# Optimization experiments

Hardware: AMD Instinct MI355X
Metric: run time of the kernel (lower is better)

Reference implementation:

```python
import jax, jax.numpy as jnp
import numpy as np

EPS = 1e-4

def _softmax_features(x, proj, is_query):
    # x: [B,H,N,D], proj: [M,D] -> features [B,H,N,M] (FAVOR+ softmax kernel)
    d = x.shape[-1]
    m = proj.shape[0]
    data_normalizer = d ** -0.25
    ratio = m ** -0.5
    xd = jnp.einsum('bhnd,md->bhnm', x * data_normalizer, proj)
    diag = 0.5 * (data_normalizer ** 2) * jnp.sum(x * x, axis=-1, keepdims=True)  # [B,H,N,1]
    if is_query:
        mx = jax.lax.stop_gradient(jnp.max(xd, axis=-1, keepdims=True))
    else:
        mx = jax.lax.stop_gradient(jnp.max(xd, axis=(-1, -2), keepdims=True))
    return ratio * (jnp.exp(xd - diag - mx) + EPS)

def setup_inputs() -> dict:
    key = jax.random.key(0)
    kq, kk, kv, kp = jax.random.split(key, 4)
    B, H, N, D, M = 4, 8, 8192, 64, 256
    Q = jax.random.normal(kq, (B, H, N, D), dtype=jnp.float32)
    K = jax.random.normal(kk, (B, H, N, D), dtype=jnp.float32)
    V = jax.random.normal(kv, (B, H, N, D), dtype=jnp.float32)
    mask = jnp.ones((B, N), dtype=jnp.float32)
    proj = jax.random.normal(kp, (M, D), dtype=jnp.float32)
    return {'Q': Q, 'K': K, 'V': V, 'mask': mask, 'proj': proj}

def reference(Q, K, V, mask, proj):
    # Mask keys/values before the kernel, as in the torch module
    Km = K * mask[:, None, :, None]
    Vm = V * mask[:, None, :, None]
    q = _softmax_features(Q, proj, is_query=True)    # [B,H,N,M]
    k = _softmax_features(Km, proj, is_query=False)  # [B,H,N,M]
    # Non-causal linear attention: out = q (k^T v) / (q k_sum)
    k_sum = jnp.sum(k, axis=-2)                         # [B,H,M]
    d_inv = 1.0 / jnp.einsum('bhnm,bhm->bhn', q, k_sum)  # [B,H,N]
    ctx = jnp.einsum('bhnm,bhnd->bhmd', k, Vm)            # [B,H,M,D]
    out = jnp.einsum('bhnm,bhmd,bhn->bhnd', q, ctx, d_inv)
    return out
```

## Files before the change

kernel.cpp:

```cpp
#include <hip/hip_runtime.h>


typedef __attribute__((ext_vector_type(8))) short short8;
typedef __attribute__((ext_vector_type(8))) _Float16 half8;
typedef __attribute__((ext_vector_type(4))) float f32x4;

namespace {
constexpr int BN = 8192, DD = 64, MM = 256, NHEADS = 32;
constexpr float CNORM = 0.35355339059327373f;
constexpr float LOG2E = 1.4426950408889634f;
constexpr float DGC   = 0.34657359027997264f;
constexpr float FEPS  = 1e-4f;
constexpr float INV2048 = 4.8828125e-4f;
constexpr int FFS = 260;

constexpr size_t OFF_BX    = 0;
constexpr size_t OFF_CS    = 8192;
constexpr size_t OFF_KSUMP = 270336;
constexpr size_t OFF_KSUMG = 335872;
constexpr size_t OFF_VSP   = 344320;
constexpr size_t OFF_CTXP  = 360704;
}

__device__ __forceinline__ unsigned short f2bf(float f) {
  unsigned u = __float_as_uint(f);
  u += 0x7fffu + ((u >> 16) & 1u);
  return (unsigned short)(u >> 16);
}
__device__ __forceinline__ float bf2f(unsigned short h) {
  return __uint_as_float(((unsigned)h) << 16);
}
__device__ __forceinline__ unsigned pk2(unsigned short a, unsigned short b) {
  return (unsigned)a | ((unsigned)b << 16);
}
__device__ __forceinline__ unsigned short f2h(float f) {
  _Float16 h = (_Float16)f;
  return __builtin_bit_cast(unsigned short, h);
}
__device__ __forceinline__ float exp2hw(float x) {
  float r;
  asm("v_exp_f32 %0, %1" : "=v"(r) : "v"(x));
  return r;
}
__device__ __forceinline__ unsigned cvtpk(float lo, float hi) {
  unsigned r;
  asm("v_cvt_pk_bf16_f32 %0, %1, %2" : "=v"(r) : "v"(lo), "v"(hi));
  return r;
}

template <int T>
__device__ __forceinline__ void xcd_map(int& bh, int& tile) {
  int id = blockIdx.y * T + blockIdx.x;
  int xcd = id & 7, s = id >> 3;
  bh = xcd * 4 + s / T;
  tile = s % T;
}

__global__ void kPrep(const float* __restrict__ proj, unsigned short* __restrict__ BxG) {
  int s = blockIdx.x * 256 + threadIdx.x;
  int l = s & 63, kb = (s >> 6) & 1, mt = s >> 7;
  int n = mt * 16 + (l & 15);
  int k0 = kb * 32 + (l >> 4) * 8;
  unsigned short o[8];
#pragma unroll
  for (int j = 0; j < 8; ++j) o[j] = f2h(proj[n * 64 + k0 + j]);
  *(uint4*)(BxG + (size_t)s * 8) =
      make_uint4(pk2(o[0], o[1]), pk2(o[2], o[3]), pk2(o[4], o[5]), pk2(o[6], o[7]));
}

__global__ void __launch_bounds__(512, 4)
kCtx(const float* __restrict__ Kin, const float* __restrict__ Vin,
     const float* __restrict__ mask, const unsigned short* __restrict__ BxG,
     float* __restrict__ ctxp, float* __restrict__ ksump,
     float* __restrict__ mxg, float* __restrict__ vsp) {
  __shared__ __align__(16) unsigned short BxH[8192];
  __shared__ __align__(16) unsigned short Fs[128 * 140];
  __shared__ __align__(16) unsigned short VF[16 * 64 * 8];
  __shared__ float wmax[8];
  __shared__ float ksred[1024];
  __shared__ float vred[512];
  const int tid = threadIdx.x;
  int bh, tl16;
  xcd_map<16>(bh, tl16);
  const int tile = tl16 >> 1, mh = tl16 & 1;
  const int b = bh >> 3;
  const float* Kh = Kin + (size_t)bh * BN * DD;
  const float* Vh = Vin + (size_t)bh * BN * DD;
  const float* mrow = mask + (size_t)b * BN;
#pragma unroll
  for (int i = 0; i < 2; ++i)
    ((uint4*)BxH)[tid + i * 512] = ((const uint4*)BxG)[mh * 1024 + tid + i * 512];
  const int w = tid >> 6, l = tid & 63, lm = l & 15, kl = l >> 4;
  const int lmv = tid & 15, klnv = (tid >> 4) & 3, dtv = (tid >> 6) & 3, ksv0 = tid >> 8;

  f32x4 cacc[4];
#pragma unroll
  for (int dt = 0; dt < 4; ++dt) cacc[dt] = f32x4{0.f, 0.f, 0.f, 0.f};
  float kspart[8] = {0.f, 0.f, 0.f, 0.f, 0.f, 0.f, 0.f, 0.f};
  float wm = -3e38f, vsum = 0.f;

  const int rbase = tile * 1024;
  float4 kv0, kv1, kv2, kv3;
  float mskK;
  {
    const float* rp = Kh + (size_t)(rbase + w * 16 + lm) * 64 + kl * 8;
    kv0 = *(const float4*)rp;        kv1 = *(const float4*)(rp + 4);
    kv2 = *(const float4*)(rp + 32); kv3 = *(const float4*)(rp + 36);
    mskK = mrow[rbase + w * 16 + lm];
  }
  __syncthreads();

  for (int ch = 0; ch < 8; ++ch) {
    const int r0 = rbase + ch * 128;
    half8 ah0, ah1, al0, al1;
    float diagv;
    {
      float scale = CNORM * LOG2E * mskK;
      float x[16] = {kv0.x, kv0.y, kv0.z, kv0.w, kv1.x, kv1.y, kv1.z, kv1.w,
                     kv2.x, kv2.y, kv2.z, kv2.w, kv3.x, kv3.y, kv3.z, kv3.w};
      float sq = 0.f;
#pragma unroll
      for (int e = 0; e < 16; ++e) {
        float y = x[e] * scale;
        _Float16 h = (_Float16)y;
        _Float16 lo = (_Float16)((y - (float)h) * 2048.0f);
        if (e < 8) { ah0[e] = h; al0[e] = lo; } else { ah1[e - 8] = h; al1[e - 8] = lo; }
        sq = fmaf(y, y, sq);
      }
      sq += __shfl_xor(sq, 16);
      sq += __shfl_xor(sq, 32);
      diagv = DGC * sq;
    }
    {
      const int nr = rbase + ((ch + 1) & 7) * 128 + w * 16 + lm;
      const float* rp = Kh + (size_t)nr * 64 + kl * 8;
      kv0 = *(const float4*)rp;        kv1 = *(const float4*)(rp + 4);
      kv2 = *(const float4*)(rp + 32); kv3 = *(const float4*)(rp + 36);
      mskK = mrow[nr];
    }
    float vv[16];
#pragma unroll
    for (int h = 0; h < 2; ++h) {
      int nb = (ksv0 * 2 + h) * 32 + klnv * 8;
#pragma unroll
      for (int j = 0; j < 8; ++j)
        vv[h * 8 + j] = Vh[(size_t)(r0 + nb + j) * 64 + dtv * 16 + lmv];
    }
    float dgv[4];
#pragma unroll
    for (int r = 0; r < 4; ++r)
      dgv[r] = __shfl(diagv, (l & 48) + kl * 4 + r);
#pragma unroll
    for (int j = 0; j < 8; ++j) {
      half8 b0 = *(const half8*)&BxH[((j * 2 + 0) * 64 + l) * 8];
      half8 b1 = *(const half8*)&BxH[((j * 2 + 1) * 64 + l) * 8];
      f32x4 a0 = {0.f, 0.f, 0.f, 0.f}, a1 = {0.f, 0.f, 0.f, 0.f};
      a0 = __builtin_amdgcn_mfma_f32_16x16x32_f16(ah0, b0, a0, 0, 0, 0);
      a0 = __builtin_amdgcn_mfma_f32_16x16x32_f16(ah1, b1, a0, 0, 0, 0);
      a1 = __builtin_amdgcn_mfma_f32_16x16x32_f16(al0, b0, a1, 0, 0, 0);
      a1 = __builtin_amdgcn_mfma_f32_16x16x32_f16(al1, b1, a1, 0, 0, 0);
      float x0 = fmaf(a1[0], INV2048, a0[0]);
      float x1 = fmaf(a1[1], INV2048, a0[1]);
      float x2 = fmaf(a1[2], INV2048, a0[2]);
      float x3 = fmaf(a1[3], INV2048, a0[3]);
      wm = fmaxf(wm, fmaxf(fmaxf(x0, x1), fmaxf(x2, x3)));
      float f0 = exp2hw(x0 - dgv[0]);
      float f1 = exp2hw(x1 - dgv[1]);
      float f2 = exp2hw(x2 - dgv[2]);
      float f3 = exp2hw(x3 - dgv[3]);
      kspart[j] += f0 + f1 + f2 + f3;
      *(uint2*)&Fs[(j * 16 + lm) * 140 + w * 16 + kl * 4] =
          make_uint2(cvtpk(f0, f1), cvtpk(f2, f3));
    }
#pragma unroll
    for (int h = 0; h < 2; ++h) {
      int ks = ksv0 * 2 + h;
      int nb = ks * 32 + klnv * 8;
      float4 m0 = *(const float4*)&mrow[r0 + nb];
      float4 m1 = *(const float4*)&mrow[r0 + nb + 4];
      float mk[8] = {m0.x, m0.y, m0.z, m0.w, m1.x, m1.y, m1.z, m1.w};
      float vm[8];
#pragma unroll
      for (int j = 0; j < 8; ++j) {
        vm[j] = vv[h * 8 + j] * mk[j];
        vsum += vm[j];
      }
      *(uint4*)&VF[((ks * 4 + dtv) * 64 + klnv * 16 + lmv) * 8] =
          make_uint4(cvtpk(vm[0], vm[1]), cvtpk(vm[2], vm[3]),
                     cvtpk(vm[4], vm[5]), cvtpk(vm[6], vm[7]));
    }
    __syncthreads();
#pragma unroll
    for (int ks = 0; ks < 4; ++ks) {
      union { short8 v; uint2 u[2]; } af;
      const int ab = (w * 16 + lm) * 140 + ks * 32 + kl * 8;
      af.u[0] = *(const uint2*)&Fs[ab];
      af.u[1] = *(const uint2*)&Fs[ab + 4];
#pragma unroll
      for (int dt = 0; dt < 4; ++dt) {
        short8 vb = *(const short8*)&VF[((ks * 4 + dt) * 64 + l) * 8];
        cacc[dt] = __builtin_amdgcn_mfma_f32_16x16x32_bf16(af.v, vb, cacc[dt], 0, 0, 0);
      }
    }
    __syncthreads();
  }
#pragma unroll
  for (int j = 0; j < 8; ++j) {
    kspart[j] += __shfl_xor(kspart[j], 16);
    kspart[j] += __shfl_xor(kspart[j], 32);
  }
  if (l < 16) {
#pragma unroll
    for (int j = 0; j < 8; ++j) ksred[(j * 16 + l) * 8 + w] = kspart[j];
  }
  {
    wm = fmaxf(wm, __shfl_xor(wm, 1));  wm = fmaxf(wm, __shfl_xor(wm, 2));
    wm = fmaxf(wm, __shfl_xor(wm, 4));  wm = fmaxf(wm, __shfl_xor(wm, 8));
    wm = fmaxf(wm, __shfl_xor(wm, 16)); wm = fmaxf(wm, __shfl_xor(wm, 32));
    if (l == 0) wmax[w] = wm;
  }
  vred[tid] = vsum;
  __syncthreads();
  if (tid < 128) {
    float s = 0.f;
#pragma unroll
    for (int k = 0; k < 8; ++k) s += ksred[tid * 8 + k];
    ksump[(size_t)(bh * 16 + tl16) * 128 + tid] = s;
  }
  if (mh == 0 && tid < 64) {
    float vs = 0.f;
#pragma unroll
    for (int k = 0; k < 8; ++k)
      vs += vred[(k >> 2) * 256 + (tid >> 4) * 64 + (k & 3) * 16 + (tid & 15)];
    vsp[(size_t)(bh * 8 + tile) * 64 + tid] = vs;
  }
  if (tid == 0) {
    float bm = wmax[0];
#pragma unroll
    for (int i = 1; i < 8; ++i) bm = fmaxf(bm, wmax[i]);
    mxg[bh * 256 + 240 + tl16] = bm;
  }
  float* cp = ctxp + (size_t)(bh * 16 + tl16) * 8192;
#pragma unroll
  for (int dt = 0; dt < 4; ++dt)
#pragma unroll
    for (int r = 0; r < 4; ++r)
      cp[(w * 16 + kl * 4 + r) * 64 + dt * 16 + lm] = cacc[dt][r];
}

__global__ void kRedCtx(const float* __restrict__ ctxp, const float* __restrict__ ksump,
                        const float* __restrict__ vsp, unsigned short* __restrict__ CsG,
                        float* __restrict__ ksumG) {
  __shared__ __align__(16) float ctxL[16384];
  __shared__ float vsL[64];
  const int bh = blockIdx.x, t = threadIdx.x;
  float MX = -3e38f;
#pragma unroll
  for (int i = 0; i < 16; ++i) MX = fmaxf(MX, ksumG[bh * 256 + 240 + i]);
  const float fsc = exp2hw(-MX);
  __syncthreads();
#pragma unroll
  for (int i = 0; i < 16; ++i) {
    int idx4 = t + i * 256;
    int mhi = (idx4 >> 11) & 1;
    int loc = idx4 & 2047;
    float4 s = make_float4(0.f, 0.f, 0.f, 0.f);
#pragma unroll
    for (int tl = 0; tl < 8; ++tl) {
      float4 a = ((const float4*)(ctxp + (size_t)(bh * 16 + tl * 2 + mhi) * 8192))[loc];
      s.x += a.x; s.y += a.y; s.z += a.z; s.w += a.w;
    }
    s.x *= fsc; s.y *= fsc; s.z *= fsc; s.w *= fsc;
    ((float4*)ctxL)[idx4] = s;
  }
  {
    int mhi = t >> 7, loc = t & 127;
    float ks = 0.f;
#pragma unroll
    for (int tl = 0; tl < 8; ++tl)
      ks += ksump[(size_t)(bh * 16 + tl * 2 + mhi) * 128 + loc];
    ksumG[bh * 256 + t] = fsc * ks + FEPS * (float)BN;
  }
  if (t < 64) {
    float vs = 0.f;
#pragma unroll
    for (int tl = 0; tl < 8; ++tl) vs += vsp[(size_t)(bh * 8 + tl) * 64 + t];
    vsL[t] = vs;
  }
  __syncthreads();
#pragma unroll
  for (int i = 0; i < 8; ++i) {
    int slot = t + i * 256;
    int l = slot & 63, s = (slot >> 6) & 7, dt = slot >> 9;
    int d = dt * 16 + (l & 15);
    int mb = s * 32 + (l >> 4) * 8;
    float ve = FEPS * vsL[d];
    unsigned short o[8];
#pragma unroll
    for (int j = 0; j < 8; ++j) o[j] = f2bf(ctxL[(mb + j) * 64 + d] + ve);
    *(uint4*)(CsG + (size_t)bh * 16384 + (size_t)slot * 8) =
        make_uint4(pk2(o[0], o[1]), pk2(o[2], o[3]), pk2(o[4], o[5]), pk2(o[6], o[7]));
  }
}

__global__ void __launch_bounds__(256, 2)
kOut(const float* __restrict__ Qin, const unsigned short* __restrict__ BxG,
     const unsigned short* __restrict__ CsG, const float* __restrict__ ksumG,
     float* __restrict__ outp) {
  __shared__ __align__(16) unsigned short BxH[16384];
  __shared__ __align__(16) unsigned short Ff[64 * FFS];
  __shared__ float den[64];
  const int tid = threadIdx.x;
  int bh, tile;
  xcd_map<32>(bh, tile);
  const float* Qh = Qin + (size_t)bh * BN * DD;
  const unsigned short* CsB = CsG + (size_t)bh * 16384;
  const int w = tid >> 6, l = tid & 63, lm = l & 15, kl = l >> 4;
#pragma unroll
  for (int i = 0; i < 16; ++i)
    ((uint4*)BxH)[tid + i * 256] = ((const uint4*)BxG)[tid + i * 256];
  short8 cb[8];
#pragma unroll
  for (int s = 0; s < 8; ++s)
    cb[s] = *(const short8*)(CsB + (size_t)(((w * 8 + s) * 64 + l) * 8));
  float kss[16];
#pragma unroll
  for (int j = 0; j < 16; ++j) kss[j] = ksumG[bh * 256 + j * 16 + lm];
  float4 qv0, qv1, qv2, qv3;
  {
    const float* rp = Qh + (size_t)(tile * 256 + w * 16 + lm) * 64 + kl * 8;
    qv0 = *(const float4*)rp;        qv1 = *(const float4*)(rp + 4);
    qv2 = *(const float4*)(rp + 32); qv3 = *(const float4*)(rp + 36);
  }
  __syncthreads();

  for (int ch = 0; ch < 4; ++ch) {
    const int r0 = tile * 256 + ch * 64;
    half8 ah0, ah1, al0, al1;
    float sq = 0.f;
    {
      const float scale = CNORM * LOG2E;
      float x[16] = {qv0.x, qv0.y, qv0.z, qv0.w, qv1.x, qv1.y, qv1.z, qv1.w,
                     qv2.x, qv2.y, qv2.z, qv2.w, qv3.x, qv3.y, qv3.z, qv3.w};
#pragma unroll
      for (int e = 0; e < 16; ++e) {
        float y = x[e] * scale;
        _Float16 h = (_Float16)y;
        _Float16 lo = (_Float16)((y - (float)h) * 2048.0f);
        if (e < 8) { ah0[e] = h; al0[e] = lo; } else { ah1[e - 8] = h; al1[e - 8] = lo; }
        sq = fmaf(y, y, sq);
      }
      sq += __shfl_xor(sq, 16);
      sq += __shfl_xor(sq, 32);
    }
    const float diagv = DGC * sq;
    {
      const int nr = tile * 256 + ((ch + 1) & 3) * 64 + w * 16 + lm;
      const float* rp = Qh + (size_t)nr * 64 + kl * 8;
      qv0 = *(const float4*)rp;        qv1 = *(const float4*)(rp + 4);
      qv2 = *(const float4*)(rp + 32); qv3 = *(const float4*)(rp + 36);
    }
    f32x4 accC[16];
#pragma unroll
    for (int j = 0; j < 16; ++j) {
      half8 b0 = *(const half8*)&BxH[((j * 2 + 0) * 64 + l) * 8];
      half8 b1 = *(const half8*)&BxH[((j * 2 + 1) * 64 + l) * 8];
      f32x4 acc0 = {0.f, 0.f, 0.f, 0.f}, acc1 = {0.f, 0.f, 0.f, 0.f};
      acc0 = __builtin_amdgcn_mfma_f32_16x16x32_f16(ah0, b0, acc0, 0, 0, 0);
      acc0 = __builtin_amdgcn_mfma_f32_16x16x32_f16(ah1, b1, acc0, 0, 0, 0);
      acc1 = __builtin_amdgcn_mfma_f32_16x16x32_f16(al0, b0, acc1, 0, 0, 0);
      acc1 = __builtin_amdgcn_mfma_f32_16x16x32_f16(al1, b1, acc1, 0, 0, 0);
#pragma unroll
      for (int r = 0; r < 4; ++r) accC[j][r] = fmaf(acc1[r], INV2048, acc0[r]);
    }
    float mrow[4];
#pragma unroll
    for (int r = 0; r < 4; ++r) {
      float m0 = accC[0][r];
#pragma unroll
      for (int j = 1; j < 16; ++j) m0 = fmaxf(m0, accC[j][r]);
      m0 = fmaxf(m0, __shfl_xor(m0, 1));
      m0 = fmaxf(m0, __shfl_xor(m0, 2));
      m0 = fmaxf(m0, __shfl_xor(m0, 4));
      m0 = fmaxf(m0, __shfl_xor(m0, 8));
      mrow[r] = m0;
    }
    float dgv[4], dnn[4] = {0.f, 0.f, 0.f, 0.f};
#pragma unroll
    for (int r = 0; r < 4; ++r)
      dgv[r] = __shfl(diagv, (l & 48) + kl * 4 + r) + mrow[r];
#pragma unroll
    for (int j = 0; j < 16; ++j) {
#pragma unroll
      for (int r = 0; r < 4; ++r) {
        float q = exp2hw(accC[j][r] - dgv[r]) + FEPS;
        unsigned short qh = f2bf(q);
        Ff[(w * 16 + kl * 4 + r) * FFS + j * 16 + lm] = qh;
        dnn[r] += bf2f(qh) * kss[j];
      }
    }
#pragma unroll
    for (int r = 0; r < 4; ++r) {
      dnn[r] += __shfl_xor(dnn[r], 1); dnn[r] += __shfl_xor(dnn[r], 2);
      dnn[r] += __shfl_xor(dnn[r], 4); dnn[r] += __shfl_xor(dnn[r], 8);
    }
    if (lm == 0) {
#pragma unroll
      for (int r = 0; r < 4; ++r) den[w * 16 + kl * 4 + r] = 1.0f / dnn[r];
    }
    __syncthreads();
    f32x4 oacc[4];
#pragma unroll
    for (int fr = 0; fr < 4; ++fr) oacc[fr] = f32x4{0.f, 0.f, 0.f, 0.f};
#pragma unroll
    for (int s = 0; s < 8; ++s) {
#pragma unroll
      for (int fr = 0; fr < 4; ++fr) {
        short8 af = *(const short8*)&Ff[(fr * 16 + lm) * FFS + s * 32 + kl * 8];
        oacc[fr] = __builtin_amdgcn_mfma_f32_16x16x32_bf16(af, cb[s], oacc[fr], 0, 0, 0);
      }
    }
#pragma unroll
    for (int fr = 0; fr < 4; ++fr) {
#pragma unroll
      for (int r = 0; r < 4; ++r) {
        int n = fr * 16 + kl * 4 + r;
        outp[((size_t)bh * BN + r0 + n) * 64 + w * 16 + lm] = oacc[fr][r] * den[n];
      }
    }
    __syncthreads();
  }
}

extern "C" void kernel_launch(void* const* d_in, const int* in_sizes, int n_in,
                              void* d_out, int out_size, void* d_ws, size_t ws_size,
                              hipStream_t stream) {
  const float* Q    = (const float*)d_in[0];
  const float* K    = (const float*)d_in[1];
  const float* V    = (const float*)d_in[2];
  const float* mask = (const float*)d_in[3];
  const float* proj = (const float*)d_in[4];
  float* out = (float*)d_out;
  float* ws = (float*)d_ws;

  unsigned short* wBx = (unsigned short*)(ws + OFF_BX);
  unsigned short* wCs = (unsigned short*)(ws + OFF_CS);
  float* wKsump = ws + OFF_KSUMP;
  float* wKsumG = ws + OFF_KSUMG;
  float* wVsp   = ws + OFF_VSP;
  float* wCtxp  = ws + OFF_CTXP;

  kPrep<<<8, 256, 0, stream>>>(proj, wBx);
  kCtx<<<dim3(16, NHEADS), 512, 0, stream>>>(K, V, mask, wBx, wCtxp, wKsump, wKsumG, wVsp);
  kRedCtx<<<NHEADS, 256, 0, stream>>>(wCtxp, wKsump, wVsp, wCs, wKsumG);
  kOut<<<dim3(32, NHEADS), 256, 0, stream>>>(Q, wBx, wCs, wKsumG, out);
}
```

Measured before the change: 129.0 us.

## Split kCtx feature dimension into four quarters to double grid size

Each kCtx block now handles a 64-wide quarter of the random-feature dimension instead of a 128-wide half, so the grid doubles to 32x32 blocks. Each wave computes half the d-tiles of the context MFMA, which also reduces per-block LDS and registers. The cost is that every K and V chunk is loaded and its diagonal recomputed by twice as many blocks, raising redundant global traffic. kRedCtx is updated to reduce over the new partial layout.

```diff
diff --git a/kernel.cpp b/kernel.cpp
--- a/kernel.cpp
+++ b/kernel.cpp
@@ -73,30 +73,29 @@
      const float* __restrict__ mask, const unsigned short* __restrict__ BxG,
      float* __restrict__ ctxp, float* __restrict__ ksump,
      float* __restrict__ mxg, float* __restrict__ vsp) {
-  __shared__ __align__(16) unsigned short BxH[8192];
-  __shared__ __align__(16) unsigned short Fs[128 * 140];
+  __shared__ __align__(16) unsigned short BxH[4096];
+  __shared__ __align__(16) unsigned short Fs[64 * 140];
   __shared__ __align__(16) unsigned short VF[16 * 64 * 8];
   __shared__ float wmax[8];
-  __shared__ float ksred[1024];
+  __shared__ float ksred[512];
   __shared__ float vred[512];
   const int tid = threadIdx.x;
-  int bh, tl16;
-  xcd_map<16>(bh, tl16);
-  const int tile = tl16 >> 1, mh = tl16 & 1;
+  int bh, tl32;
+  xcd_map<32>(bh, tl32);
+  const int tile = tl32 >> 2, q = tl32 & 3;
   const int b = bh >> 3;
   const float* Kh = Kin + (size_t)bh * BN * DD;
   const float* Vh = Vin + (size_t)bh * BN * DD;
   const float* mrow = mask + (size_t)b * BN;
-#pragma unroll
-  for (int i = 0; i < 2; ++i)
-    ((uint4*)BxH)[tid + i * 512] = ((const uint4*)BxG)[mh * 1024 + tid + i * 512];
+  ((uint4*)BxH)[tid] = ((const uint4*)BxG)[q * 512 + tid];
   const int w = tid >> 6, l = tid & 63, lm = l & 15, kl = l >> 4;
   const int lmv = tid & 15, klnv = (tid >> 4) & 3, dtv = (tid >> 6) & 3, ksv0 = tid >> 8;
-
-  f32x4 cacc[4];
-#pragma unroll
-  for (int dt = 0; dt < 4; ++dt) cacc[dt] = f32x4{0.f, 0.f, 0.f, 0.f};
-  float kspart[8] = {0.f, 0.f, 0.f, 0.f, 0.f, 0.f, 0.f, 0.f};
+  const int mg = w & 3, dh = w >> 2;
+
+  f32x4 cacc[2];
+  cacc[0] = f32x4{0.f, 0.f, 0.f, 0.f};
+  cacc[1] = f32x4{0.f, 0.f, 0.f, 0.f};
+  float kspart[4] = {0.f, 0.f, 0.f, 0.f};
   float wm = -3e38f, vsum = 0.f;
 
   const int rbase = tile * 1024;
@@ -151,7 +150,7 @@
     for (int r = 0; r < 4; ++r)
       dgv[r] = __shfl(diagv, (l & 48) + kl * 4 + r);
 #pragma unroll
-    for (int j = 0; j < 8; ++j) {
+    for (int j = 0; j < 4; ++j) {
       half8 b0 = *(const half8*)&BxH[((j * 2 + 0) * 64 + l) * 8];
       half8 b1 = *(const half8*)&BxH[((j * 2 + 1) * 64 + l) * 8];
       f32x4 a0 = {0.f, 0.f, 0.f, 0.f}, a1 = {0.f, 0.f, 0.f, 0.f};
@@ -193,25 +192,26 @@
 #pragma unroll
     for (int ks = 0; ks < 4; ++ks) {
       union { short8 v; uint2 u[2]; } af;
-      const int ab = (w * 16 + lm) * 140 + ks * 32 + kl * 8;
+      const int ab = (mg * 16 + lm) * 140 + ks * 32 + kl * 8;
       af.u[0] = *(const uint2*)&Fs[ab];
       af.u[1] = *(const uint2*)&Fs[ab + 4];
 #pragma unroll
-      for (int dt = 0; dt < 4; ++dt) {
+      for (int dtp = 0; dtp < 2; ++dtp) {
+        int dt = dh * 2 + dtp;
         short8 vb = *(const short8*)&VF[((ks * 4 + dt) * 64 + l) * 8];
-        cacc[dt] = __builtin_amdgcn_mfma_f32_16x16x32_bf16(af.v, vb, cacc[dt], 0, 0, 0);
+        cacc[dtp] = __builtin_amdgcn_mfma_f32_16x16x32_bf16(af.v, vb, cacc[dtp], 0, 0, 0);
       }
     }
     __syncthreads();
   }
 #pragma unroll
-  for (int j = 0; j < 8; ++j) {
+  for (int j = 0; j < 4; ++j) {
     kspart[j] += __shfl_xor(kspart[j], 16);
     kspart[j] += __shfl_xor(kspart[j], 32);
   }
   if (l < 16) {
 #pragma unroll
-    for (int j = 0; j < 8; ++j) ksred[(j * 16 + l) * 8 + w] = kspart[j];
+    for (int j = 0; j < 4; ++j) ksred[(j * 16 + l) * 8 + w] = kspart[j];
   }
   {
     wm = fmaxf(wm, __shfl_xor(wm, 1));  wm = fmaxf(wm, __shfl_xor(wm, 2));
@@ -221,13 +221,13 @@
   }
   vred[tid] = vsum;
   __syncthreads();
-  if (tid < 128) {
+  if (tid < 64) {
     float s = 0.f;
 #pragma unroll
     for (int k = 0; k < 8; ++k) s += ksred[tid * 8 + k];
-    ksump[(size_t)(bh * 16 + tl16) * 128 + tid] = s;
-  }
-  if (mh == 0 && tid < 64) {
+    ksump[(size_t)(bh * 32 + tl32) * 64 + tid] = s;
+  }
+  if (q == 0 && tid < 64) {
     float vs = 0.f;
 #pragma unroll
     for (int k = 0; k < 8; ++k)
@@ -238,14 +238,14 @@
     float bm = wmax[0];
 #pragma unroll
     for (int i = 1; i < 8; ++i) bm = fmaxf(bm, wmax[i]);
-    mxg[bh * 256 + 240 + tl16] = bm;
-  }
-  float* cp = ctxp + (size_t)(bh * 16 + tl16) * 8192;
-#pragma unroll
-  for (int dt = 0; dt < 4; ++dt)
+    mxg[bh * 256 + 224 + tl32] = bm;
+  }
+  float* cp = ctxp + (size_t)(bh * 32 + tl32) * 4096;
+#pragma unroll
+  for (int dtp = 0; dtp < 2; ++dtp)
 #pragma unroll
     for (int r = 0; r < 4; ++r)
-      cp[(w * 16 + kl * 4 + r) * 64 + dt * 16 + lm] = cacc[dt][r];
+      cp[(mg * 16 + kl * 4 + r) * 64 + (dh * 2 + dtp) * 16 + lm] = cacc[dtp][r];
 }
 
 __global__ void kRedCtx(const float* __restrict__ ctxp, const float* __restrict__ ksump,
@@ -256,29 +256,29 @@
   const int bh = blockIdx.x, t = threadIdx.x;
   float MX = -3e38f;
 #pragma unroll
-  for (int i = 0; i < 16; ++i) MX = fmaxf(MX, ksumG[bh * 256 + 240 + i]);
+  for (int i = 0; i < 32; ++i) MX = fmaxf(MX, ksumG[bh * 256 + 224 + i]);
   const float fsc = exp2hw(-MX);
   __syncthreads();
 #pragma unroll
   for (int i = 0; i < 16; ++i) {
     int idx4 = t + i * 256;
-    int mhi = (idx4 >> 11) & 1;
-    int loc = idx4 & 2047;
+    int qq = (idx4 >> 10) & 3;
+    int loc = idx4 & 1023;
     float4 s = make_float4(0.f, 0.f, 0.f, 0.f);
 #pragma unroll
     for (int tl = 0; tl < 8; ++tl) {
-      float4 a = ((const float4*)(ctxp + (size_t)(bh * 16 + tl * 2 + mhi) * 8192))[loc];
+      float4 a = ((const float4*)(ctxp + (size_t)(bh * 32 + tl * 4 + qq) * 4096))[loc];
       s.x += a.x; s.y += a.y; s.z += a.z; s.w += a.w;
     }
     s.x *= fsc; s.y *= fsc; s.z *= fsc; s.w *= fsc;
     ((float4*)ctxL)[idx4] = s;
   }
   {
-    int mhi = t >> 7, loc = t & 127;
+    int qq = t >> 6, loc = t & 63;
     float ks = 0.f;
 #pragma unroll
     for (int tl = 0; tl < 8; ++tl)
-      ks += ksump[(size_t)(bh * 16 + tl * 2 + mhi) * 128 + loc];
+      ks += ksump[(size_t)(bh * 32 + tl * 4 + qq) * 64 + loc];
     ksumG[bh * 256 + t] = fsc * ks + FEPS * (float)BN;
   }
   if (t < 64) {
@@ -451,7 +451,7 @@
   float* wCtxp  = ws + OFF_CTXP;
 
   kPrep<<<8, 256, 0, stream>>>(proj, wBx);
-  kCtx<<<dim3(16, NHEADS), 512, 0, stream>>>(K, V, mask, wBx, wCtxp, wKsump, wKsumG, wVsp);
+  kCtx<<<dim3(32, NHEADS), 512, 0, stream>>>(K, V, mask, wBx, wCtxp, wKsump, wKsumG, wVsp);
   kRedCtx<<<NHEADS, 256, 0, stream>>>(wCtxp, wKsump, wVsp, wCs, wKsumG);
   kOut<<<dim3(32, NHEADS), 256, 0, stream>>>(Q, wBx, wCs, wKsumG, out);
 }
```

After: 147.3 us. +14.2%, slower.
